# Kernel tuning notes

Measured on AMD Instinct MI355X. Metric: run time of the kernel, lower is better.

The kernel has to match this reference:

```python
import jax, jax.numpy as jnp
import numpy as np

B, Hs, Ws, C = 4, 56, 56, 128
NH, K = 4, 7


def _layernorm(x, w, b, eps=1e-5):
    mu = jnp.mean(x, axis=-1, keepdims=True)
    var = jnp.mean((x - mu) ** 2, axis=-1, keepdims=True)
    return (x - mu) * jax.lax.rsqrt(var + eps) * w + b


def setup_inputs() -> dict:
    key = jax.random.key(0)
    ks = jax.random.split(key, 16)
    s = lambda k_, shape, fan: jax.random.normal(k_, shape, jnp.float32) * (fan ** -0.5)
    hid = 4 * C
    return {
        "x": jax.random.normal(ks[0], (B, Hs, Ws, C), jnp.float32),
        "norm1_w": jnp.ones((C,), jnp.float32),
        "norm1_b": jnp.zeros((C,), jnp.float32),
        "qkv_w": s(ks[1], (3 * C, C), C),
        "qkv_b": jnp.zeros((3 * C,), jnp.float32),
        "rpb": 0.02 * jax.random.normal(ks[2], (NH, 2 * K - 1, 2 * K - 1), jnp.float32),
        "proj_w": s(ks[3], (C, C), C),
        "proj_b": jnp.zeros((C,), jnp.float32),
        "norm2_w": jnp.ones((C,), jnp.float32),
        "norm2_b": jnp.zeros((C,), jnp.float32),
        "fc1_w": s(ks[4], (hid, C), C),
        "fc1_b": jnp.zeros((hid,), jnp.float32),
        "fc2_w": s(ks[5], (C, hid), hid),
        "fc2_b": jnp.zeros((C,), jnp.float32),
    }


def _neighborhood_attention(x, qkv_w, qkv_b, rpb, proj_w, proj_b):
    # x: [B, H, W, C]; NATTEN-style clamped sliding-window attention.
    b, h, w, c = x.shape
    nh = rpb.shape[0]
    k = (rpb.shape[1] + 1) // 2
    hd = c // nh
    scale = hd ** -0.5

    # static clamped window start indices (windows shifted to stay in-bounds)
    sh = np.clip(np.arange(h) - k // 2, 0, h - k)
    sw = np.clip(np.arange(w) - k // 2, 0, w - k)
    idx_h = sh[:, None] + np.arange(k)                  # [H, k]
    idx_w = sw[:, None] + np.arange(k)                  # [W, k]
    bias_h = idx_h - np.arange(h)[:, None] + (k - 1)    # [H, k] in [0, 2k-2]
    bias_w = idx_w - np.arange(w)[:, None] + (k - 1)    # [W, k]

    qkv = x @ qkv_w.T + qkv_b                           # [B,H,W,3C]
    qkv = qkv.reshape(b, h, w, 3, nh, hd)
    q = qkv[..., 0, :, :] * scale                       # [B,H,W,nh,hd]
    kk = qkv[..., 1, :, :]
    vv = qkv[..., 2, :, :]

    # gather neighborhood keys/values: [B,H,kh,W,kw,nh,hd]
    k_win = kk[:, idx_h][:, :, :, idx_w]
    v_win = vv[:, idx_h][:, :, :, idx_w]

    # attention scores + relative positional bias
    scores = jnp.einsum('bhwnd,bhiwjnd->bnhwij', q, k_win)   # [B,nh,H,W,kh,kw]
    bias = rpb[:, bias_h][:, :, :, bias_w]                   # [nh,H,kh,W,kw]
    bias = jnp.transpose(bias, (0, 1, 3, 2, 4))              # [nh,H,W,kh,kw]
    scores = scores + bias[None]

    attn = jax.nn.softmax(scores.reshape(b, nh, h, w, k * k), axis=-1)
    attn = attn.reshape(b, nh, h, w, k, k)
    out = jnp.einsum('bnhwij,bhiwjnd->bhwnd', attn, v_win)   # [B,H,W,nh,hd]
    out = out.reshape(b, h, w, c)
    return out @ proj_w.T + proj_b


def reference(x, norm1_w, norm1_b, qkv_w, qkv_b, rpb, proj_w, proj_b,
              norm2_w, norm2_b, fc1_w, fc1_b, fc2_w, fc2_b):
    # attention block (pre-norm, residual)
    y = _layernorm(x, norm1_w, norm1_b)
    y = _neighborhood_attention(y, qkv_w, qkv_b, rpb, proj_w, proj_b)
    x = x + y
    # MLP block
    z = _layernorm(x, norm2_w, norm2_b)
    z = jax.nn.gelu(z @ fc1_w.T + fc1_b, approximate=False)
    z = z @ fc2_w.T + fc2_b
    return x + z
```

## Files before the change

kernel.cpp:

```cpp
#include <hip/hip_runtime.h>
#include <math.h>

#define TOK 12544
#define CDIM 128
#define NHEAD 4
#define HD 32
#define KS 7
#define HSZ 56
#define WSZ 56

typedef __attribute__((ext_vector_type(8))) short short8;
typedef __attribute__((ext_vector_type(4))) float f32x4;

__device__ inline ushort f2b(float f) {
    uint u = __float_as_uint(f);
    u += 0x7fffu + ((u >> 16) & 1u);
    return (ushort)(u >> 16);
}

__global__ void convert_w(const float* __restrict__ a, const float* __restrict__ b,
                          const float* __restrict__ c, const float* __restrict__ d,
                          ushort* __restrict__ wb) {
    int e = (blockIdx.x * 256 + threadIdx.x) * 4;
    const float* src;
    if (e < 49152)       src = a + e;
    else if (e < 65536)  src = b + (e - 49152);
    else if (e < 131072) src = c + (e - 65536);
    else                 src = d + (e - 131072);
    float4 v = *(const float4*)src;
    uint2 pk;
    pk.x = (uint)f2b(v.x) | ((uint)f2b(v.y) << 16);
    pk.y = (uint)f2b(v.z) | ((uint)f2b(v.w) << 16);
    *(uint2*)(wb + e) = pk;
}

__device__ inline void ln_to_lds(const float* __restrict__ X, int m0,
                                 const float* __restrict__ lnw, const float* __restrict__ lnb,
                                 ushort* __restrict__ lds) {
    int wv = threadIdx.x >> 6, lane = threadIdx.x & 63;
    #pragma unroll
    for (int r = 0; r < 8; r++) {
        int rl = wv * 8 + r;
        float2 v = *(const float2*)(X + (size_t)(m0 + rl) * CDIM + lane * 2);
        float s = v.x + v.y;
        #pragma unroll
        for (int o = 32; o > 0; o >>= 1) s += __shfl_xor(s, o);
        float mu = s * (1.0f / 128.0f);
        float d0 = v.x - mu, d1 = v.y - mu;
        float sq = d0 * d0 + d1 * d1;
        #pragma unroll
        for (int o = 32; o > 0; o >>= 1) sq += __shfl_xor(sq, o);
        float rstd = rsqrtf(sq * (1.0f / 128.0f) + 1e-5f);
        float2 wv2 = *(const float2*)(lnw + lane * 2);
        float2 bv2 = *(const float2*)(lnb + lane * 2);
        uint pk = (uint)f2b(d0 * rstd * wv2.x + bv2.x)
                | ((uint)f2b(d1 * rstd * wv2.y + bv2.y) << 16);
        *(uint*)((char*)lds + rl * 256 + ((lane * 4) ^ ((rl & 7) << 4))) = pk;
    }
}

__global__ __launch_bounds__(512) void ln1_qkv(const float* __restrict__ X,
                                               const ushort* __restrict__ W,
                                               const float* __restrict__ bias,
                                               const float* __restrict__ lnw,
                                               const float* __restrict__ lnb,
                                               ushort* __restrict__ Y) {
    __shared__ ushort xn[64 * 128];
    int m0 = blockIdx.x * 64;
    ln_to_lds(X, m0, lnw, lnb, xn);
    __syncthreads();

    int wv = threadIdx.x >> 6, lane = threadIdx.x & 63;
    int lr = lane & 15, kg = lane >> 4;
    int n0 = wv * 48;
    f32x4 acc[4][3] = {};
    #pragma unroll
    for (int k0 = 0; k0 < 128; k0 += 32) {
        short8 bf[3];
        #pragma unroll
        for (int ni = 0; ni < 3; ni++)
            bf[ni] = *(const short8*)(W + (size_t)(n0 + ni * 16 + lr) * 128 + k0 + kg * 8);
        #pragma unroll
        for (int mg = 0; mg < 4; mg++) {
            int row = mg * 16 + lr;
            short8 a0 = *(const short8*)((char*)xn + row * 256 + ((k0 * 2 + kg * 16) ^ ((row & 7) << 4)));
            #pragma unroll
            for (int ni = 0; ni < 3; ni++)
                acc[mg][ni] = __builtin_amdgcn_mfma_f32_16x16x32_bf16(a0, bf[ni], acc[mg][ni], 0, 0, 0);
        }
    }
    #pragma unroll
    for (int mg = 0; mg < 4; mg++)
    #pragma unroll
    for (int ni = 0; ni < 3; ni++) {
        int col = n0 + ni * 16 + lr;
        float bn = bias[col];
        #pragma unroll
        for (int r = 0; r < 4; r++) {
            int row = m0 + mg * 16 + kg * 4 + r;
            float v = acc[mg][ni][r] + bn;
            if (col < CDIM) v *= 0.17677669529663687f;
            Y[(size_t)row * 384 + col] = f2b(v);
        }
    }
}

__global__ __launch_bounds__(512) void proj_mlp(const ushort* __restrict__ aob,
                                                const ushort* __restrict__ Wp,
                                                const float* __restrict__ bp,
                                                const float* __restrict__ X,
                                                const ushort* __restrict__ W1,
                                                const float* __restrict__ b1,
                                                const ushort* __restrict__ W2,
                                                const float* __restrict__ b2,
                                                const float* __restrict__ lnw,
                                                const float* __restrict__ lnb,
                                                float* __restrict__ out) {
    __shared__ float  x2f[64 * 132];
    __shared__ ushort zn[64 * 128];
    __shared__ ushort hb[64 * 256];
    int m0 = blockIdx.x * 64;
    int wv = threadIdx.x >> 6, lane = threadIdx.x & 63;
    int lr = lane & 15, kg = lane >> 4;

    {
        int n0 = wv * 16;
        f32x4 accp[4] = {};
        #pragma unroll
        for (int k0 = 0; k0 < 128; k0 += 32) {
            short8 bf = *(const short8*)(Wp + (size_t)(n0 + lr) * 128 + k0 + kg * 8);
            #pragma unroll
            for (int mg = 0; mg < 4; mg++) {
                short8 a0 = *(const short8*)(aob + (size_t)(m0 + mg * 16 + lr) * 128 + k0 + kg * 8);
                accp[mg] = __builtin_amdgcn_mfma_f32_16x16x32_bf16(a0, bf, accp[mg], 0, 0, 0);
            }
        }
        float bn = bp[n0 + lr];
        #pragma unroll
        for (int mg = 0; mg < 4; mg++)
        #pragma unroll
        for (int r = 0; r < 4; r++) {
            int row = mg * 16 + kg * 4 + r;
            x2f[row * 132 + n0 + lr] = accp[mg][r] + bn
                                     + X[(size_t)(m0 + row) * CDIM + n0 + lr];
        }
    }
    __syncthreads();

    #pragma unroll
    for (int r = 0; r < 8; r++) {
        int rl = wv * 8 + r;
        float2 v = *(const float2*)&x2f[rl * 132 + lane * 2];
        float s = v.x + v.y;
        #pragma unroll
        for (int o = 32; o > 0; o >>= 1) s += __shfl_xor(s, o);
        float mu = s * (1.0f / 128.0f);
        float d0 = v.x - mu, d1 = v.y - mu;
        float sq = d0 * d0 + d1 * d1;
        #pragma unroll
        for (int o = 32; o > 0; o >>= 1) sq += __shfl_xor(sq, o);
        float rstd = rsqrtf(sq * (1.0f / 128.0f) + 1e-5f);
        float2 wv2 = *(const float2*)(lnw + lane * 2);
        float2 bv2 = *(const float2*)(lnb + lane * 2);
        uint pk = (uint)f2b(d0 * rstd * wv2.x + bv2.x)
                | ((uint)f2b(d1 * rstd * wv2.y + bv2.y) << 16);
        *(uint*)((char*)zn + rl * 256 + ((lane * 4) ^ ((rl & 7) << 4))) = pk;
    }

    int rw0 = (wv >> 2) * 32, cw0 = (wv & 3) * 32;
    f32x4 acc2[2][2] = {};
    __syncthreads();

    #pragma unroll
    for (int p = 0; p < 2; p++) {
        f32x4 acc1[4][2] = {};
        int nc0 = wv * 32;
        #pragma unroll
        for (int k0 = 0; k0 < 128; k0 += 32) {
            short8 bf[2];
            #pragma unroll
            for (int ni = 0; ni < 2; ni++)
                bf[ni] = *(const short8*)(W1 + (size_t)(p * 256 + nc0 + ni * 16 + lr) * 128 + k0 + kg * 8);
            #pragma unroll
            for (int mg = 0; mg < 4; mg++) {
                int row = mg * 16 + lr;
                short8 a0 = *(const short8*)((char*)zn + row * 256 + ((k0 * 2 + kg * 16) ^ ((row & 7) << 4)));
                #pragma unroll
                for (int ni = 0; ni < 2; ni++)
                    acc1[mg][ni] = __builtin_amdgcn_mfma_f32_16x16x32_bf16(a0, bf[ni], acc1[mg][ni], 0, 0, 0);
            }
        }
        #pragma unroll
        for (int mg = 0; mg < 4; mg++)
        #pragma unroll
        for (int ni = 0; ni < 2; ni++) {
            int lc = nc0 + ni * 16 + lr;
            float bn = b1[p * 256 + lc];
            #pragma unroll
            for (int r = 0; r < 4; r++) {
                int row = mg * 16 + kg * 4 + r;
                float v = acc1[mg][ni][r] + bn;
                float t = v + 0.044715f * v * v * v;
                float sg = 1.0f / (1.0f + __expf(-1.5957691216f * t));
                v = v * sg;
                *(ushort*)((char*)hb + row * 512 + ((lc * 2) ^ ((row & 7) << 4))) = f2b(v);
            }
        }
        __syncthreads();

        #pragma unroll
        for (int k0 = 0; k0 < 256; k0 += 32) {
            short8 a0[2], bf[2];
            #pragma unroll
            for (int mi = 0; mi < 2; mi++) {
                int row = rw0 + mi * 16 + lr;
                a0[mi] = *(const short8*)((char*)hb + row * 512 + ((k0 * 2 + kg * 16) ^ ((row & 7) << 4)));
            }
            #pragma unroll
            for (int ni = 0; ni < 2; ni++)
                bf[ni] = *(const short8*)(W2 + (size_t)(cw0 + ni * 16 + lr) * 512 + p * 256 + k0 + kg * 8);
            #pragma unroll
            for (int mi = 0; mi < 2; mi++)
            #pragma unroll
            for (int ni = 0; ni < 2; ni++)
                acc2[mi][ni] = __builtin_amdgcn_mfma_f32_16x16x32_bf16(a0[mi], bf[ni], acc2[mi][ni], 0, 0, 0);
        }
        __syncthreads();
    }

    #pragma unroll
    for (int mi = 0; mi < 2; mi++)
    #pragma unroll
    for (int ni = 0; ni < 2; ni++) {
        int col = cw0 + ni * 16 + lr;
        float bn = b2[col];
        #pragma unroll
        for (int r = 0; r < 4; r++) {
            int row = rw0 + mi * 16 + kg * 4 + r;
            out[(size_t)(m0 + row) * CDIM + col] = acc2[mi][ni][r] + bn + x2f[row * 132 + col];
        }
    }
}

__global__ __launch_bounds__(256) void nat_attn6(const ushort* __restrict__ qkv,
                                                 const float* __restrict__ rpb,
                                                 ushort* __restrict__ ao) {
    __shared__ ushort katt[8704];
    __shared__ ushort vs[32 * 232];
    __shared__ float rpl[169];
    ushort* ks = katt;

    int tid = threadIdx.x, wv = tid >> 6, lane = tid & 63;
    int lr = lane & 15, kg = lane >> 4;
    int bid = blockIdx.x;
    int blk = (bid & 7) * 98 + (bid >> 3);
    int tile = blk % 49, hb2 = blk / 49;
    int head = hb2 & 3, b = hb2 >> 2;
    int r0 = (tile / 7) * 8, c0 = (tile % 7) * 8;
    int hr0 = min(max(r0 - 3, 0), HSZ - 14);
    int hc0 = min(max(c0 - 3, 0), WSZ - 14);
    int bimg = b * HSZ * WSZ;

    if (tid < 169) rpl[tid] = rpb[head * 169 + tid];
    for (int idx = tid; idx < 784; idx += 256) {
        int t = idx >> 2, c = idx & 3;
        int gtok = bimg + (hr0 + t / 14) * WSZ + hc0 + t % 14;
        short8 v = *(const short8*)(qkv + (size_t)gtok * 384 + 128 + head * HD + c * 8);
        *(short8*)(ks + t * 32 + ((c ^ (t & 3)) << 3)) = v;
    }
    for (int idx = tid; idx < 392; idx += 256) {
        int pr = idx >> 2, c = idx & 3;
        int t = pr * 2;
        int gtok = bimg + (hr0 + t / 14) * WSZ + hc0 + t % 14;
        const ushort* vp = qkv + (size_t)gtok * 384 + 256 + head * HD + c * 8;
        short8 v0 = *(const short8*)vp;
        short8 v1 = *(const short8*)(vp + 384);
        #pragma unroll
        for (int q = 0; q < 8; q++)
            *(uint*)(vs + (c * 8 + q) * 232 + t) =
                (uint)(ushort)v0[q] | ((uint)(ushort)v1[q] << 16);
    }
    for (int idx = tid; idx < 32 * 18; idx += 256)
        *(uint*)(vs + (idx / 18) * 232 + 196 + (idx % 18) * 2) = 0;
    __syncthreads();

    int i0 = r0 + 2 * wv;
    int hw0 = min(max(i0 - 3, 0), HSZ - KS);
    int dwr = hw0 - hr0;
    int tbase = dwr * 14;
    int rb = tbase & ~7;
    int rboff = tbase - rb;

    int lpix = lr;
    int agp = bimg + (r0 + 2 * wv + (lpix >> 3)) * WSZ + c0 + (lpix & 7);
    short8 aq = *(const short8*)(qkv + (size_t)agp * 384 + head * HD + kg * 8);
    f32x4 sc[7];
    #pragma unroll
    for (int tl = 0; tl < 7; tl++) {
        int t = tbase + tl * 16 + lr;
        short8 bk = *(const short8*)(ks + t * 32 + ((kg ^ (t & 3)) << 3));
        f32x4 z = {0.f, 0.f, 0.f, 0.f};
        sc[tl] = __builtin_amdgcn_mfma_f32_16x16x32_bf16(aq, bk, z, 0, 0, 0);
    }
    __syncthreads();

    ushort* attw = katt + wv * 16 * 136;
    #pragma unroll
    for (int z = 0; z < 16; z++) {
        int ii = z * 64 + lane;
        *(uint*)(attw + (ii >> 6) * 136 + (ii & 63) * 2) = 0;
    }
    float inv[4];
    #pragma unroll
    for (int r = 0; r < 4; r++) {
        int idx = kg * 4 + r;
        int i = r0 + 2 * wv + (idx >> 3), j = c0 + (idx & 7);
        int shh = min(max(i - 3, 0), HSZ - KS);
        int sww = min(max(j - 3, 0), WSZ - KS);
        int dih = shh - hr0, dj = sww - hc0;
        int offh = hr0 - i + 6, offw = hc0 - j + 6;
        float sv[7];
        float mx = -1e30f;
        #pragma unroll
        for (int tl = 0; tl < 7; tl++) {
            int t = tbase + tl * 16 + lr;
            int thr = (unsigned)t / 14u;
            int twr = t - thr * 14;
            bool in = ((unsigned)(thr - dih) < 7u) && ((unsigned)(twr - dj) < 7u);
            int bidx = (thr + offh) * 13 + (twr + offw);
            bidx = min(max(bidx, 0), 168);
            float s = sc[tl][r] + rpl[bidx];
            sv[tl] = in ? s : -1e30f;
            mx = fmaxf(mx, sv[tl]);
        }
        #pragma unroll
        for (int o = 8; o > 0; o >>= 1) mx = fmaxf(mx, __shfl_xor(mx, o));
        float sum = 0.f;
        #pragma unroll
        for (int tl = 0; tl < 7; tl++) {
            float e = __expf(sv[tl] - mx);
            sum += e;
            attw[idx * 136 + rboff + tl * 16 + lr] = f2b(e);
        }
        #pragma unroll
        for (int o = 8; o > 0; o >>= 1) sum += __shfl_xor(sum, o);
        inv[r] = 1.0f / sum;
    }

    f32x4 po[2] = {};
    #pragma unroll
    for (int kst = 0; kst < 4; kst++) {
        short8 pa = *(const short8*)(attw + lr * 136 + kst * 32 + kg * 8);
        #pragma unroll
        for (int n = 0; n < 2; n++) {
            short8 vb = *(const short8*)(vs + (n * 16 + lr) * 232 + rb + kst * 32 + kg * 8);
            po[n] = __builtin_amdgcn_mfma_f32_16x16x32_bf16(pa, vb, po[n], 0, 0, 0);
        }
    }

    #pragma unroll
    for (int n = 0; n < 2; n++)
    #pragma unroll
    for (int rr = 0; rr < 4; rr++) {
        int idx = kg * 4 + rr;
        int gp = bimg + (r0 + 2 * wv + (idx >> 3)) * WSZ + c0 + (idx & 7);
        ao[(size_t)gp * CDIM + head * HD + n * 16 + lr] = f2b(po[n][rr] * inv[rr]);
    }
}

extern "C" void kernel_launch(void* const* d_in, const int* in_sizes, int n_in,
                              void* d_out, int out_size, void* d_ws, size_t ws_size,
                              hipStream_t stream) {
    const float* x      = (const float*)d_in[0];
    const float* n1w    = (const float*)d_in[1];
    const float* n1b    = (const float*)d_in[2];
    const float* qkv_w  = (const float*)d_in[3];
    const float* qkv_b  = (const float*)d_in[4];
    const float* rpb    = (const float*)d_in[5];
    const float* proj_w = (const float*)d_in[6];
    const float* proj_b = (const float*)d_in[7];
    const float* n2w    = (const float*)d_in[8];
    const float* n2b    = (const float*)d_in[9];
    const float* fc1_w  = (const float*)d_in[10];
    const float* fc1_b  = (const float*)d_in[11];
    const float* fc2_w  = (const float*)d_in[12];
    const float* fc2_b  = (const float*)d_in[13];
    float* out = (float*)d_out;

    ushort* wb   = (ushort*)d_ws;
    ushort* qkvb = wb + 196608;
    ushort* aob  = qkvb + (size_t)TOK * 384;

    const ushort* w_qkv  = wb;
    const ushort* w_proj = wb + 49152;
    const ushort* w_fc1  = wb + 65536;
    const ushort* w_fc2  = wb + 131072;

    convert_w<<<192, 256, 0, stream>>>(qkv_w, proj_w, fc1_w, fc2_w, wb);
    ln1_qkv<<<TOK / 64, 512, 0, stream>>>(x, w_qkv, qkv_b, n1w, n1b, qkvb);
    nat_attn6<<<4 * NHEAD * 49, 256, 0, stream>>>(qkvb, rpb, aob);
    proj_mlp<<<TOK / 64, 512, 0, stream>>>(aob, w_proj, proj_b, x,
                                           w_fc1, fc1_b, w_fc2, fc2_b, n2w, n2b, out);
}
```

Measured before the change: 59.11 us.

## Halve row tile to 32 tokens with 256-thread blocks in QKV and MLP kernels

Both ln1_qkv and proj_mlp now process 32 tokens per block with 4 waves instead of 64 tokens with 8 waves. Each wave covers a wider column slice so the per-wave MFMA tiling is reshaped. This doubles the grid to 392 blocks, which fills the CUs better, and halves LDS use per block. In exchange, weights are reloaded twice as often per token and each wave holds more accumulators, which raises register pressure.

```diff
diff --git a/kernel.cpp b/kernel.cpp
--- a/kernel.cpp
+++ b/kernel.cpp
@@ -34,9 +34,9 @@
     *(uint2*)(wb + e) = pk;
 }
 
-__device__ inline void ln_to_lds(const float* __restrict__ X, int m0,
-                                 const float* __restrict__ lnw, const float* __restrict__ lnb,
-                                 ushort* __restrict__ lds) {
+__device__ inline void ln_to_lds32(const float* __restrict__ X, int m0,
+                                   const float* __restrict__ lnw, const float* __restrict__ lnb,
+                                   ushort* __restrict__ lds) {
     int wv = threadIdx.x >> 6, lane = threadIdx.x & 63;
     #pragma unroll
     for (int r = 0; r < 8; r++) {
@@ -59,40 +59,40 @@
     }
 }
 
-__global__ __launch_bounds__(512) void ln1_qkv(const float* __restrict__ X,
+__global__ __launch_bounds__(256) void ln1_qkv(const float* __restrict__ X,
                                                const ushort* __restrict__ W,
                                                const float* __restrict__ bias,
                                                const float* __restrict__ lnw,
                                                const float* __restrict__ lnb,
                                                ushort* __restrict__ Y) {
-    __shared__ ushort xn[64 * 128];
-    int m0 = blockIdx.x * 64;
-    ln_to_lds(X, m0, lnw, lnb, xn);
+    __shared__ ushort xn[32 * 128];
+    int m0 = blockIdx.x * 32;
+    ln_to_lds32(X, m0, lnw, lnb, xn);
     __syncthreads();
 
     int wv = threadIdx.x >> 6, lane = threadIdx.x & 63;
     int lr = lane & 15, kg = lane >> 4;
-    int n0 = wv * 48;
-    f32x4 acc[4][3] = {};
+    int n0 = wv * 96;
+    f32x4 acc[2][6] = {};
     #pragma unroll
     for (int k0 = 0; k0 < 128; k0 += 32) {
-        short8 bf[3];
-        #pragma unroll
-        for (int ni = 0; ni < 3; ni++)
+        short8 bf[6];
+        #pragma unroll
+        for (int ni = 0; ni < 6; ni++)
             bf[ni] = *(const short8*)(W + (size_t)(n0 + ni * 16 + lr) * 128 + k0 + kg * 8);
         #pragma unroll
-        for (int mg = 0; mg < 4; mg++) {
+        for (int mg = 0; mg < 2; mg++) {
             int row = mg * 16 + lr;
             short8 a0 = *(const short8*)((char*)xn + row * 256 + ((k0 * 2 + kg * 16) ^ ((row & 7) << 4)));
             #pragma unroll
-            for (int ni = 0; ni < 3; ni++)
+            for (int ni = 0; ni < 6; ni++)
                 acc[mg][ni] = __builtin_amdgcn_mfma_f32_16x16x32_bf16(a0, bf[ni], acc[mg][ni], 0, 0, 0);
         }
     }
     #pragma unroll
-    for (int mg = 0; mg < 4; mg++)
-    #pragma unroll
-    for (int ni = 0; ni < 3; ni++) {
+    for (int mg = 0; mg < 2; mg++)
+    #pragma unroll
+    for (int ni = 0; ni < 6; ni++) {
         int col = n0 + ni * 16 + lr;
         float bn = bias[col];
         #pragma unroll
@@ -105,7 +105,7 @@
     }
 }
 
-__global__ __launch_bounds__(512) void proj_mlp(const ushort* __restrict__ aob,
+__global__ __launch_bounds__(256) void proj_mlp(const ushort* __restrict__ aob,
                                                 const ushort* __restrict__ Wp,
                                                 const float* __restrict__ bp,
                                                 const float* __restrict__ X,
@@ -116,33 +116,42 @@
                                                 const float* __restrict__ lnw,
                                                 const float* __restrict__ lnb,
                                                 float* __restrict__ out) {
-    __shared__ float  x2f[64 * 132];
-    __shared__ ushort zn[64 * 128];
-    __shared__ ushort hb[64 * 256];
-    int m0 = blockIdx.x * 64;
+    __shared__ float  x2f[32 * 132];
+    __shared__ ushort zn[32 * 128];
+    __shared__ ushort hb[32 * 256];
+    int m0 = blockIdx.x * 32;
     int wv = threadIdx.x >> 6, lane = threadIdx.x & 63;
     int lr = lane & 15, kg = lane >> 4;
 
     {
-        int n0 = wv * 16;
-        f32x4 accp[4] = {};
+        int n0 = wv * 32;
+        f32x4 accp[2][2] = {};
         #pragma unroll
         for (int k0 = 0; k0 < 128; k0 += 32) {
-            short8 bf = *(const short8*)(Wp + (size_t)(n0 + lr) * 128 + k0 + kg * 8);
-            #pragma unroll
-            for (int mg = 0; mg < 4; mg++) {
+            short8 bf[2];
+            #pragma unroll
+            for (int ni = 0; ni < 2; ni++)
+                bf[ni] = *(const short8*)(Wp + (size_t)(n0 + ni * 16 + lr) * 128 + k0 + kg * 8);
+            #pragma unroll
+            for (int mg = 0; mg < 2; mg++) {
                 short8 a0 = *(const short8*)(aob + (size_t)(m0 + mg * 16 + lr) * 128 + k0 + kg * 8);
-                accp[mg] = __builtin_amdgcn_mfma_f32_16x16x32_bf16(a0, bf, accp[mg], 0, 0, 0);
+                #pragma unroll
+                for (int ni = 0; ni < 2; ni++)
+                    accp[mg][ni] = __builtin_amdgcn_mfma_f32_16x16x32_bf16(a0, bf[ni], accp[mg][ni], 0, 0, 0);
             }
         }
-        float bn = bp[n0 + lr];
-        #pragma unroll
-        for (int mg = 0; mg < 4; mg++)
-        #pragma unroll
-        for (int r = 0; r < 4; r++) {
-            int row = mg * 16 + kg * 4 + r;
-            x2f[row * 132 + n0 + lr] = accp[mg][r] + bn
-                                     + X[(size_t)(m0 + row) * CDIM + n0 + lr];
+        #pragma unroll
+        for (int mg = 0; mg < 2; mg++)
+        #pragma unroll
+        for (int ni = 0; ni < 2; ni++) {
+            int col = n0 + ni * 16 + lr;
+            float bn = bp[col];
+            #pragma unroll
+            for (int r = 0; r < 4; r++) {
+                int row = mg * 16 + kg * 4 + r;
+                x2f[row * 132 + col] = accp[mg][ni][r] + bn
+                                     + X[(size_t)(m0 + row) * CDIM + col];
+            }
         }
     }
     __syncthreads();
@@ -167,33 +176,33 @@
         *(uint*)((char*)zn + rl * 256 + ((lane * 4) ^ ((rl & 7) << 4))) = pk;
     }
 
-    int rw0 = (wv >> 2) * 32, cw0 = (wv & 3) * 32;
-    f32x4 acc2[2][2] = {};
+    int rw0 = (wv >> 1) * 16, cw0 = (wv & 1) * 64;
+    f32x4 acc2[4] = {};
     __syncthreads();
 
     #pragma unroll
     for (int p = 0; p < 2; p++) {
-        f32x4 acc1[4][2] = {};
-        int nc0 = wv * 32;
+        f32x4 acc1[2][4] = {};
+        int nc0 = wv * 64;
         #pragma unroll
         for (int k0 = 0; k0 < 128; k0 += 32) {
-            short8 bf[2];
-            #pragma unroll
-            for (int ni = 0; ni < 2; ni++)
+            short8 bf[4];
+            #pragma unroll
+            for (int ni = 0; ni < 4; ni++)
                 bf[ni] = *(const short8*)(W1 + (size_t)(p * 256 + nc0 + ni * 16 + lr) * 128 + k0 + kg * 8);
             #pragma unroll
-            for (int mg = 0; mg < 4; mg++) {
+            for (int mg = 0; mg < 2; mg++) {
                 int row = mg * 16 + lr;
                 short8 a0 = *(const short8*)((char*)zn + row * 256 + ((k0 * 2 + kg * 16) ^ ((row & 7) << 4)));
                 #pragma unroll
-                for (int ni = 0; ni < 2; ni++)
+                for (int ni = 0; ni < 4; ni++)
                     acc1[mg][ni] = __builtin_amdgcn_mfma_f32_16x16x32_bf16(a0, bf[ni], acc1[mg][ni], 0, 0, 0);
             }
         }
         #pragma unroll
-        for (int mg = 0; mg < 4; mg++)
-        #pragma unroll
-        for (int ni = 0; ni < 2; ni++) {
+        for (int mg = 0; mg < 2; mg++)
+        #pragma unroll
+        for (int ni = 0; ni < 4; ni++) {
             int lc = nc0 + ni * 16 + lr;
             float bn = b1[p * 256 + lc];
             #pragma unroll
@@ -210,34 +219,25 @@
 
         #pragma unroll
         for (int k0 = 0; k0 < 256; k0 += 32) {
-            short8 a0[2], bf[2];
-            #pragma unroll
-            for (int mi = 0; mi < 2; mi++) {
-                int row = rw0 + mi * 16 + lr;
-                a0[mi] = *(const short8*)((char*)hb + row * 512 + ((k0 * 2 + kg * 16) ^ ((row & 7) << 4)));
+            int row = rw0 + lr;
+            short8 a0 = *(const short8*)((char*)hb + row * 512 + ((k0 * 2 + kg * 16) ^ ((row & 7) << 4)));
+            #pragma unroll
+            for (int ni = 0; ni < 4; ni++) {
+                short8 bf = *(const short8*)(W2 + (size_t)(cw0 + ni * 16 + lr) * 512 + p * 256 + k0 + kg * 8);
+                acc2[ni] = __builtin_amdgcn_mfma_f32_16x16x32_bf16(a0, bf, acc2[ni], 0, 0, 0);
             }
-            #pragma unroll
-            for (int ni = 0; ni < 2; ni++)
-                bf[ni] = *(const short8*)(W2 + (size_t)(cw0 + ni * 16 + lr) * 512 + p * 256 + k0 + kg * 8);
-            #pragma unroll
-            for (int mi = 0; mi < 2; mi++)
-            #pragma unroll
-            for (int ni = 0; ni < 2; ni++)
-                acc2[mi][ni] = __builtin_amdgcn_mfma_f32_16x16x32_bf16(a0[mi], bf[ni], acc2[mi][ni], 0, 0, 0);
         }
         __syncthreads();
     }
 
     #pragma unroll
-    for (int mi = 0; mi < 2; mi++)
-    #pragma unroll
-    for (int ni = 0; ni < 2; ni++) {
+    for (int ni = 0; ni < 4; ni++) {
         int col = cw0 + ni * 16 + lr;
         float bn = b2[col];
         #pragma unroll
         for (int r = 0; r < 4; r++) {
-            int row = rw0 + mi * 16 + kg * 4 + r;
-            out[(size_t)(m0 + row) * CDIM + col] = acc2[mi][ni][r] + bn + x2f[row * 132 + col];
+            int row = rw0 + kg * 4 + r;
+            out[(size_t)(m0 + row) * CDIM + col] = acc2[ni][r] + bn + x2f[row * 132 + col];
         }
     }
 }
@@ -397,8 +397,8 @@
     const ushort* w_fc2  = wb + 131072;
 
     convert_w<<<192, 256, 0, stream>>>(qkv_w, proj_w, fc1_w, fc2_w, wb);
-    ln1_qkv<<<TOK / 64, 512, 0, stream>>>(x, w_qkv, qkv_b, n1w, n1b, qkvb);
+    ln1_qkv<<<TOK / 32, 256, 0, stream>>>(x, w_qkv, qkv_b, n1w, n1b, qkvb);
     nat_attn6<<<4 * NHEAD * 49, 256, 0, stream>>>(qkvb, rpb, aob);
-    proj_mlp<<<TOK / 64, 512, 0, stream>>>(aob, w_proj, proj_b, x,
+    proj_mlp<<<TOK / 32, 256, 0, stream>>>(aob, w_proj, proj_b, x,
                                            w_fc1, fc1_b, w_fc2, fc2_b, n2w, n2b, out);
 }
```

Result: slower. 68.73 us (+16.3%).
